# Kernel optimization log

Measured on AMD Instinct MI355X. Metric: run time of the kernel, lower is better.

## Reference

```python
import jax, jax.numpy as jnp
import numpy as np

EPS = 1e-5


def conv3d(x, w):
    # x: [N, C, D, H, W], w: [O, I, kD, kH, kW]; SAME padding emulates the
    # densified coordinate-expanding sparse conv on a fixed grid.
    return jax.lax.conv_general_dilated(
        x, w, window_strides=(1, 1, 1), padding='SAME',
        dimension_numbers=('NCDHW', 'OIDHW', 'NCDHW'))


def bn(x, gamma, beta, mean, var):
    # eval-mode batchnorm, fused scale/shift
    scale = gamma * jax.lax.rsqrt(var + EPS)          # [C]
    shift = beta - mean * scale                       # [C]
    return x * scale[None, :, None, None, None] + shift[None, :, None, None, None]


def setup_inputs() -> dict:
    key = jax.random.key(0)
    ks = jax.random.split(key, 20)
    C = 16
    D, H, W = 128, 128, 16

    def w(k, shape, fan):
        return jax.random.normal(k, shape, dtype=jnp.float32) / np.sqrt(fan)

    inp = {}
    inp['x'] = jax.random.normal(ks[0], (1, C, D, H, W), dtype=jnp.float32)
    inp['w1'] = w(ks[1], (C, C, 3, 3, 1), C * 9)
    inp['w2'] = w(ks[2], (C, C, 3, 3, 1), C * 9)
    inp['w3'] = w(ks[3], (C, C, 5, 5, 3), C * 75)
    inp['w4'] = w(ks[4], (C, C, 7, 7, 5), C * 245)
    inp['w5'] = w(ks[5], (C, C, 3, 3, 1), C * 9)
    inp['w6'] = w(ks[6], (C, C, 5, 5, 3), C * 75)
    inp['w7'] = w(ks[7], (C, C, 7, 7, 5), C * 245)
    inp['wch'] = w(ks[8], (C, C, 1, 1, 1), C)
    inp['wr1'] = w(ks[9], (C, C, 3, 3, 1), C * 9)
    inp['wr2'] = w(ks[10], (C, C, 5, 5, 3), C * 75)
    inp['wr3'] = w(ks[11], (C, C, 7, 7, 5), C * 245)
    # 10 BN layers: bn_1..bn_7 -> rows 0..6, bn_res_1..3 -> rows 7..9
    inp['bn_gamma'] = jax.random.uniform(ks[12], (10, C), dtype=jnp.float32) + 0.5
    inp['bn_beta'] = 0.1 * jax.random.normal(ks[13], (10, C), dtype=jnp.float32)
    inp['bn_mean'] = 0.1 * jax.random.normal(ks[14], (10, C), dtype=jnp.float32)
    inp['bn_var'] = jax.random.uniform(ks[15], (10, C), dtype=jnp.float32) + 0.5
    return inp


def reference(x, w1, w2, w3, w4, w5, w6, w7, wch, wr1, wr2, wr3,
              bn_gamma, bn_beta, bn_mean, bn_var):
    def cbn(h, w_, i):
        return bn(conv3d(h, w_), bn_gamma[i], bn_beta[i], bn_mean[i], bn_var[i])

    x1 = cbn(x, w1, 0)
    x2 = cbn(x1, w2, 1)
    x3 = cbn(x1, w3, 2)
    x4 = cbn(x1, w4, 3)
    t1 = jax.nn.relu(x2 + x3 + x4)
    x5 = cbn(t1, w5, 4)
    x6 = cbn(t1, w6, 5)
    x7 = cbn(t1, w7, 6)
    xs = jax.nn.relu(x1 + x2 + x3 + x4 + x5 + x6 + x7)
    y0 = conv3d(xs, wch)
    y1 = cbn(x, wr1, 7)
    y2 = cbn(x, wr2, 8)
    y3 = cbn(x, wr3, 9)
    return jax.nn.relu(x1 + y0 + y1 + y2 + y3)
```

## Files before the change

### kernel.cpp

```cpp
#include <hip/hip_runtime.h>
#include <hip/hip_bf16.h>

typedef __attribute__((ext_vector_type(8))) short short8;
typedef __attribute__((ext_vector_type(4))) short s16x4;
typedef __attribute__((ext_vector_type(4))) float f32x4;

constexpr int C  = 16;
constexpr int DD = 128, HH = 128, WW = 16;
constexpr int HW = HH * WW;
constexpr int SP = DD * HW;
constexpr int TOT = C * SP;

constexpr int WP_ = 20, HP_ = 134, DP_ = 134;
constexpr int ROWE   = WP_ * C;
constexpr int PLANEE = HP_ * ROWE;
constexpr int PADE   = DP_ * PLANEE;

using gas_ptr = const __attribute__((address_space(1))) void*;
using las_ptr = __attribute__((address_space(3))) void*;

constexpr int OFF_W1  = 0;
constexpr int OFF_WCH = 5 * 512;
constexpr int OFF_G0  = OFF_WCH + 512;
constexpr int OFF_G1  = OFF_G0 + 147 * 512;
constexpr int OFF_G2  = OFF_G1 + 147 * 512;
constexpr int WPK_TOT = OFF_G2 + 147 * 512;

constexpr int CONV_BUFSZ = 7 * 256 * 16;

__device__ __forceinline__ float bf16_to_f(short s)
{
    union { unsigned u; float f; } cv;
    cv.u = ((unsigned)(unsigned short)s) << 16;
    return cv.f;
}

template <int EP>
__device__ __forceinline__
void conv_core(int b, const short* __restrict__ xp, const short* __restrict__ wpk,
               const float* __restrict__ bias, float* __restrict__ F,
               short* __restrict__ P, char* __restrict__ smem)
{
    constexpr int KD = 7, KH = 7, KW = 5;
    constexpr int PH = 3;
    constexpr int KWP = 3;
    constexpr int NUP = (2 + KD - 1) / 2;
    constexpr int NB  = 8 + KH - 1;
    constexpr int NR  = 16 + 2 * PH;
    constexpr int NCHP = NR * 40;
    constexpr int NCH  = 2 * NCHP;

    const int dblk = b >> 3, hb = b & 7;
    const int d0   = dblk * 2;
    const int tid  = threadIdx.x;
    const int wid  = tid >> 6, lane = tid & 63;
    const int pid  = wid >> 1, m = wid & 1;
    const int l15  = lane & 15;
    const int cih  = (lane >> 4) & 1;
    const int tsel = lane >> 5;

    const char* xb = (const char*)xp;
    const char* wb = (const char*)wpk;
    const int hp0  = hb * 16;

    auto stage = [&](int buf, int up) {
#pragma unroll
        for (int it = 0; it < 7; ++it) {
            int chunk = it * 256 + tid;
            int cc = chunk < NCH ? chunk : NCH - 1;
            int pl = (cc >= NCHP) ? 1 : 0;
            int cp = cc - pl * NCHP;
            const char* g = xb
                + (size_t)((d0 + 2 * up + pl) * PLANEE + hp0 * ROWE) * 2
                + (size_t)cp * 16;
            void* l = (void*)(smem + buf * CONV_BUFSZ + (it * 256 + wid * 64) * 16);
            __builtin_amdgcn_global_load_lds((gas_ptr)g, (las_ptr)l, 16, 0, 0);
        }
    };

    f32x4 acc[2][8] = {};

    stage(0, 0);
#pragma unroll 1
    for (int up = 0; up < NUP; ++up) {
        const int cur = up & 1;
        if (up + 1 < NUP) {
            stage(cur ^ 1, up + 1);
            asm volatile("s_waitcnt vmcnt(7)" ::: "memory");
        } else {
            asm volatile("s_waitcnt vmcnt(0)" ::: "memory");
        }
        __builtin_amdgcn_s_barrier();

        const int u = 2 * up + m;
        const char* lb = smem + cur * CONV_BUFSZ + m * (NR * 640) + pid * 8 * 640;
#pragma unroll
        for (int kwp = 0; kwp < KWP; ++kwp) {
            const int kwa = 2 * kwp;
            const int kwb_ = (2 * kwp + 1 < KW) ? 2 * kwp + 1 : KW - 1;
            const unsigned laneoff =
                (unsigned)((l15 + (tsel ? kwb_ : kwa)) * 32 + cih * 16);

            short8 Bf[NB];
#pragma unroll
            for (int rB = 0; rB < NB; ++rB)
                Bf[rB] = *(const short8*)(lb + rB * 640 + laneoff);
            short8 Af[2][7];
#pragma unroll
            for (int ad = 0; ad < 2; ++ad) {
                const int kd = u - ad;
                if (kd < 0 || kd >= KD) continue;
#pragma unroll
                for (int kh = 0; kh < KH; ++kh)
                    Af[ad][kh] = *(const short8*)(
                        wb + (unsigned)(((kd * KH + kh) * KWP + kwp) * 1024 + lane * 16));
            }

            __builtin_amdgcn_s_setprio(1);
#pragma unroll
            for (int ad = 0; ad < 2; ++ad) {
                const int kd = u - ad;
                if (kd < 0 || kd >= KD) continue;
#pragma unroll
                for (int kh = 0; kh < KH; ++kh) {
#pragma unroll
                    for (int r = 0; r < 8; ++r)
                        acc[ad][r] = __builtin_amdgcn_mfma_f32_16x16x32_bf16(
                            Af[ad][kh], Bf[r + kh], acc[ad][r], 0, 0, 0);
                }
            }
            __builtin_amdgcn_s_setprio(0);
        }
        __builtin_amdgcn_s_barrier();
    }

    float* mlds = (float*)smem;
    if (m == 1) {
#pragma unroll
        for (int ad = 0; ad < 2; ++ad)
#pragma unroll
            for (int r = 0; r < 8; ++r)
                *(f32x4*)&mlds[(((pid * 2 + ad) * 8 + r) * 64 + lane) * 4] = acc[ad][r];
    }
    __syncthreads();
    if (m == 1) return;
#pragma unroll
    for (int ad = 0; ad < 2; ++ad)
#pragma unroll
        for (int r = 0; r < 8; ++r) {
            const f32x4 o = *(const f32x4*)&mlds[(((pid * 2 + ad) * 8 + r) * 64 + lane) * 4];
#pragma unroll
            for (int j = 0; j < 4; ++j) acc[ad][r][j] += o[j];
        }

    const int cb = (lane >> 4) * 4;
    const f32x4 bv = *(const f32x4*)(bias + cb);
    const int h0 = hb * 16 + pid * 8;
#pragma unroll
    for (int ad = 0; ad < 2; ++ad)
#pragma unroll
        for (int r = 0; r < 8; ++r) {
            const int d = d0 + ad, h = h0 + r;
            const unsigned fidx = (unsigned)(((d * HH + h) * WW + l15) * C + cb);
            f32x4 val;
#pragma unroll
            for (int j = 0; j < 4; ++j) val[j] = acc[ad][r][j] + bv[j];
            if (EP == 0) {
                *(f32x4*)(F + fidx) = val;
            } else if (EP == 2) {
                s16x4 sv;
#pragma unroll
                for (int j = 0; j < 4; ++j) {
                    __hip_bfloat16 hv = __float2bfloat16(fmaxf(val[j], 0.f));
                    sv[j] = *(short*)&hv;
                }
                *(s16x4*)(P + (size_t)(d + 3) * PLANEE + (h + 3) * ROWE
                          + (l15 + 2) * 16 + cb) = sv;
                *(f32x4*)(F + fidx) = val;
            } else {
                const f32x4 f2 = *(const f32x4*)(F + fidx);
                short* prow = P + (size_t)(d + 3) * PLANEE + (h + 3) * ROWE
                              + (l15 + 2) * 16 + cb;
                const s16x4 xv = *(const s16x4*)prow;
                s16x4 sv;
#pragma unroll
                for (int j = 0; j < 4; ++j) {
                    const float x1 = bf16_to_f(xv[j]);
                    __hip_bfloat16 hv = __float2bfloat16(fmaxf(x1 + val[j] + f2[j], 0.f));
                    sv[j] = *(short*)&hv;
                }
                *(s16x4*)prow = sv;
            }
        }
}

__device__ __forceinline__ int swz512(int b0)
{
    return (b0 & 7) * 64 + (b0 >> 3);
}

template <int EP>
__global__ __launch_bounds__(256, 2)
void conv_tile_lds(const short* __restrict__ xp, const short* __restrict__ wpk,
                   const float* __restrict__ bias, float* __restrict__ F,
                   short* __restrict__ P)
{
    __shared__ alignas(16) char smem[2 * CONV_BUFSZ];
    conv_core<EP>(swz512(blockIdx.x), xp, wpk, bias, F, P, smem);
}

__global__ __launch_bounds__(256, 2)
void conv_dual(const short* __restrict__ xpA, const short* __restrict__ wpkA,
               const float* __restrict__ biasA, float* __restrict__ FA,
               short* __restrict__ PA_,
               const short* __restrict__ xpB, const short* __restrict__ wpkB,
               const float* __restrict__ biasB, float* __restrict__ FB)
{
    __shared__ alignas(16) char smem[2 * CONV_BUFSZ];
    const int b0 = blockIdx.x;
    if (b0 < 512)
        conv_core<2>(swz512(b0), xpA, wpkA, biasA, FA, PA_, smem);
    else
        conv_core<0>(swz512(b0 - 512), xpB, wpkB, biasB, FB, nullptr, smem);
}

template <int KD, int KH, int KW, int NTAPS, bool WF, int PW>
__global__ __launch_bounds__(256, 4)
void conv_mfma(const short* __restrict__ xp, const short* __restrict__ wpk,
               const float* __restrict__ bn_g, const float* __restrict__ bn_b,
               const float* __restrict__ bn_m, const float* __restrict__ bn_v,
               int layer, float* __restrict__ F, short* __restrict__ P)
{
    constexpr int PD = (KD - 1) / 2, PH = (KH - 1) / 2, PW_ = (KW - 1) / 2;
    constexpr int NP = (NTAPS + 1) / 2;

    const int b    = blockIdx.x;
    const int d    = b >> 3, hb = b & 7;
    const int tid  = threadIdx.x;
    const int wid  = tid >> 6, lane = tid & 63;
    const int h0   = hb * 16 + wid * 4;

    const int l15  = lane & 15;
    const int cih  = (lane >> 4) & 1;
    const int tsel = lane >> 5;
    const unsigned laneoff = (unsigned)(l15 * 32 + cih * 16);

    unsigned off_r[4];
#pragma unroll
    for (int r = 0; r < 4; ++r) {
        const int h = h0 + r;
        off_r[r] = (unsigned)((((d + (3 - PD)) * HP_ + (h + (3 - PH))) * ROWE
                               + (2 - PW_) * C) * 2) + laneoff;
    }

    const char* xb = (const char*)xp;
    const char* wb = (const char*)wpk;

    f32x4 acc[4] = {};
#pragma unroll 2
    for (int p = 0; p < NP; ++p) {
        const int ta = 2 * p;
        const int tb = (2 * p + 1 < NTAPS) ? 2 * p + 1 : NTAPS - 1;
        const int kda = ta / (KH * KW), ra = ta % (KH * KW);
        const int kha = ra / KW,        kwa = ra % KW;
        const int kdb = tb / (KH * KW), rb = tb % (KH * KW);
        const int khb = rb / KW,        kwb = rb % KW;
        const unsigned toa = (unsigned)((kda * PLANEE + kha * ROWE + kwa * C) * 2);
        const unsigned tob = (unsigned)((kdb * PLANEE + khb * ROWE + kwb * C) * 2);
        const unsigned ts  = tsel ? tob : toa;

        const short8 a = *(const short8*)(wb + (unsigned)(p * 1024 + lane * 16));
#pragma unroll
        for (int r = 0; r < 4; ++r) {
            const short8 bf = *(const short8*)(xb + (off_r[r] + ts));
            acc[r] = __builtin_amdgcn_mfma_f32_16x16x32_bf16(a, bf, acc[r], 0, 0, 0);
        }
    }

    float sc[4], sh[4];
    const int cb = (lane >> 4) * 4;
    {
        const f32x4 g  = *(const f32x4*)(bn_g + layer * C + cb);
        const f32x4 be = *(const f32x4*)(bn_b + layer * C + cb);
        const f32x4 mm = *(const f32x4*)(bn_m + layer * C + cb);
        const f32x4 v  = *(const f32x4*)(bn_v + layer * C + cb);
#pragma unroll
        for (int j = 0; j < 4; ++j) { sc[j] = g[j] / sqrtf(v[j] + 1e-5f); sh[j] = be[j] - mm[j] * sc[j]; }
    }
#pragma unroll
    for (int r = 0; r < 4; ++r) {
        const int h = h0 + r;
        f32x4 val;
#pragma unroll
        for (int j = 0; j < 4; ++j) val[j] = acc[r][j] * sc[j] + sh[j];
        if (PW == 1) {
            s16x4 sv;
#pragma unroll
            for (int j = 0; j < 4; ++j) {
                __hip_bfloat16 hv = __float2bfloat16(val[j]);
                sv[j] = *(short*)&hv;
            }
            *(s16x4*)(P + (size_t)(d + 3) * PLANEE + (h + 3) * ROWE
                      + (l15 + 2) * 16 + cb) = sv;
        }
        if (WF) {
            float* dst = F + (unsigned)(((d * HH + h) * WW + l15) * C + cb);
            *(f32x4*)dst = val;
        }
    }
}

__global__ __launch_bounds__(256, 4)
void final_conv(const short* __restrict__ xsp, const short* __restrict__ wpk,
                const float* __restrict__ F1, float* __restrict__ out)
{
    const int b    = blockIdx.x;
    const int d    = b >> 3, hb = b & 7;
    const int tid  = threadIdx.x;
    const int wid  = tid >> 6, lane = tid & 63;
    const int h0   = hb * 16 + wid * 4;
    const int l15  = lane & 15;
    const int cih  = (lane >> 4) & 1;
    const int cb   = (lane >> 4) * 4;
    const unsigned laneoff = (unsigned)((l15 + 2) * 32 + cih * 16);

    const char* xb = (const char*)xsp;
    const short8 a = *(const short8*)((const char*)wpk + (unsigned)(lane * 16));

#pragma unroll
    for (int r = 0; r < 4; ++r) {
        const int h = h0 + r;
        const unsigned off = (unsigned)(((size_t)(d + 3) * PLANEE + (h + 3) * ROWE) * 2)
                             + laneoff;
        const short8 bf = *(const short8*)(xb + off);
        f32x4 acc = {};
        acc = __builtin_amdgcn_mfma_f32_16x16x32_bf16(a, bf, acc, 0, 0, 0);
        const f32x4 f1 = *(const f32x4*)(F1 + (unsigned)(((d * HH + h) * WW + l15) * C + cb));
#pragma unroll
        for (int j = 0; j < 4; ++j) {
            const float v = fmaxf(acc[j] + f1[j], 0.f);
            out[(unsigned)((cb + j) * SP + d * HW + h * WW + l15)] = v;
        }
    }
}

__global__ __launch_bounds__(256)
void pack_x(const float* __restrict__ x, short* __restrict__ xp,
            short* __restrict__ pa)
{
    const int b  = blockIdx.x;
    const int dp = b / HP_, hp = b % HP_;
    const int t  = threadIdx.x;
    const int d  = dp - 3, h = hp - 3;
    const bool inr = ((unsigned)d < (unsigned)DD) && ((unsigned)h < (unsigned)HH);
    short* row  = xp + (unsigned)(dp * PLANEE + hp * ROWE);
    short* rowp = pa + (unsigned)(dp * PLANEE + hp * ROWE);

    const int w = t & 15, ci = t >> 4;
    float v = 0.f;
    if (inr) v = x[ci * SP + d * HW + h * WW + w];
    __hip_bfloat16 hv = __float2bfloat16(v);
    row[(w + 2) * C + ci] = *(short*)&hv;
    if (t < 64) {
        const int pi = t >> 4;
        const int wp = (pi < 2) ? pi : (16 + pi);
        row[wp * C + (t & 15)] = 0;
    }
    if (!inr) {
        for (int i = t; i < ROWE; i += 256) rowp[i] = 0;
    } else if (t < 64) {
        const int pi = t >> 4;
        const int wp = (pi < 2) ? pi : (16 + pi);
        rowp[wp * C + (t & 15)] = 0;
    }
}

__global__ __launch_bounds__(256)
void pack_x2(const float* __restrict__ x, short* __restrict__ xp,
             short* __restrict__ pa, short* __restrict__ t1p)
{
    const int b  = blockIdx.x;
    const int dp = b / HP_, hp = b % HP_;
    const int t  = threadIdx.x;
    const int d  = dp - 3, h = hp - 3;
    const bool inr = ((unsigned)d < (unsigned)DD) && ((unsigned)h < (unsigned)HH);
    short* row  = xp  + (unsigned)(dp * PLANEE + hp * ROWE);
    short* rowp = pa  + (unsigned)(dp * PLANEE + hp * ROWE);
    short* rowt = t1p + (unsigned)(dp * PLANEE + hp * ROWE);

    const int w = t & 15, ci = t >> 4;
    float v = 0.f;
    if (inr) v = x[ci * SP + d * HW + h * WW + w];
    __hip_bfloat16 hv = __float2bfloat16(v);
    row[(w + 2) * C + ci] = *(short*)&hv;
    if (t < 64) {
        const int pi = t >> 4;
        const int wp = (pi < 2) ? pi : (16 + pi);
        row[wp * C + (t & 15)] = 0;
    }
    if (!inr) {
        for (int i = t; i < ROWE; i += 256) { rowp[i] = 0; rowt[i] = 0; }
    } else if (t < 64) {
        const int pi = t >> 4;
        const int wp = (pi < 2) ? pi : (16 + pi);
        rowp[wp * C + (t & 15)] = 0;
        rowt[wp * C + (t & 15)] = 0;
    }
}

__global__ __launch_bounds__(256)
void pack_small(const float* __restrict__ w1, const float* __restrict__ wch,
                short* __restrict__ dst)
{
    const int b = blockIdx.x;
    const int t = threadIdx.x;
    const int l = t >> 2, jj = t & 3;
    const int co = l & 15, cih = (l >> 4) & 1, tp = l >> 5;
    unsigned out = 0;
    if (b < 5) {
        const int tap = 2 * b + tp;
#pragma unroll
        for (int s = 0; s < 2; ++s) {
            const int ci = cih * 8 + jj * 2 + s;
            const float v = (tap < 9) ? w1[(co * C + ci) * 9 + tap] : 0.f;
            __hip_bfloat16 hv = __float2bfloat16(v);
            out |= ((unsigned)*(unsigned short*)&hv) << (16 * s);
        }
        ((unsigned*)(dst + OFF_W1))[b * 256 + l * 4 + jj] = out;
    } else {
#pragma unroll
        for (int s = 0; s < 2; ++s) {
            const int ci = cih * 8 + jj * 2 + s;
            const float v = (tp == 0) ? wch[co * C + ci] : 0.f;
            __hip_bfloat16 hv = __float2bfloat16(v);
            out |= ((unsigned)*(unsigned short*)&hv) << (16 * s);
        }
        ((unsigned*)(dst + OFF_WCH))[l * 4 + jj] = out;
    }
}

struct W9 { const float* p[9]; };

__global__ __launch_bounds__(256)
void pack_fused(W9 w, const float* __restrict__ w1,
                const float* __restrict__ bng, const float* __restrict__ bnb,
                const float* __restrict__ bnm, const float* __restrict__ bnv,
                short* __restrict__ dst, float* __restrict__ bias)
{
    constexpr int kDm[3] = {3, 5, 7}, kHm[3] = {3, 5, 7}, kWm[3] = {1, 3, 5};
    constexpr int KHWm[3] = {9, 75, 245};

    const int b = blockIdx.x;
    const int g = b / 147, pr = b % 147;
    const int row = pr / 3, kwp = pr % 3;
    const int kd = row / 7, kh = row % 7;
    const int t = threadIdx.x;
    const int l = t >> 2, jj = t & 3;
    const int co = l & 15, cih = (l >> 4) & 1, tp = l >> 5;
    const int kw = 2 * kwp + tp;

    unsigned out = 0;
#pragma unroll
    for (int s = 0; s < 2; ++s) {
        const int ci = cih * 8 + jj * 2 + s;
        float val = 0.f;
        if (kw < 5) {
#pragma unroll
            for (int m = 0; m < 3; ++m) {
                const int od = (7 - kDm[m]) / 2, oh = (7 - kHm[m]) / 2, ow = (5 - kWm[m]) / 2;
                const int rd = kd - od, rh = kh - oh, rw = kw - ow;
                if ((unsigned)rd < (unsigned)kDm[m] && (unsigned)rh < (unsigned)kHm[m]
                    && (unsigned)rw < (unsigned)kWm[m]) {
                    const int layer = g * 3 + m + 1;
                    const float sbn = bng[layer * C + co] / sqrtf(bnv[layer * C + co] + 1e-5f);
                    val += sbn * w.p[g * 3 + m][(co * C + ci) * KHWm[m]
                                               + (rd * kHm[m] + rh) * kWm[m] + rw];
                }
            }
            if (g == 2) {
                const int rd = kd - 2, rh = kh - 2, rw = kw - 2;
                if ((unsigned)rd < 3u && (unsigned)rh < 3u && rw == 0) {
                    const float sbn = bng[co] / sqrtf(bnv[co] + 1e-5f);
                    val += sbn * w1[(co * C + ci) * 9 + rd * 3 + rh];
                }
            }
        }
        __hip_bfloat16 hv = __float2bfloat16(val);
        out |= ((unsigned)*(unsigned short*)&hv) << (16 * s);
    }
    ((unsigned*)(dst + OFF_G0))[(g * 147 + pr) * 256 + l * 4 + jj] = out;

    if (pr == 0 && t < 16) {
        float bsum = 0.f;
#pragma unroll
        for (int m = 0; m < 3; ++m) {
            const int layer = g * 3 + m + 1;
            const float sbn = bng[layer * C + t] / sqrtf(bnv[layer * C + t] + 1e-5f);
            bsum += bnb[layer * C + t] - bnm[layer * C + t] * sbn;
        }
        if (g == 2) {
            const float sbn = bng[t] / sqrtf(bnv[t] + 1e-5f);
            bsum += bnb[t] - bnm[t] * sbn;
        }
        bias[g * 16 + t] = bsum;
    }
}

extern "C" void kernel_launch(void* const* d_in, const int* in_sizes, int n_in,
                              void* d_out, int out_size, void* d_ws, size_t ws_size,
                              hipStream_t stream)
{
    const float* x   = (const float*)d_in[0];
    const float* w1  = (const float*)d_in[1];
    const float* wch = (const float*)d_in[8];
    const float* bng = (const float*)d_in[12];
    const float* bnb = (const float*)d_in[13];
    const float* bnm = (const float*)d_in[14];
    const float* bnv = (const float*)d_in[15];

    W9 w9;
    w9.p[0] = (const float*)d_in[2];  w9.p[1] = (const float*)d_in[3];
    w9.p[2] = (const float*)d_in[4];  w9.p[3] = (const float*)d_in[5];
    w9.p[4] = (const float*)d_in[6];  w9.p[5] = (const float*)d_in[7];
    w9.p[6] = (const float*)d_in[9];  w9.p[7] = (const float*)d_in[10];
    w9.p[8] = (const float*)d_in[11];

    short* XP   = (short*)d_ws;
    short* PA   = XP + PADE;
    float* F1   = (float*)(PA + PADE);
    short* WPK  = (short*)(F1 + TOT);
    float* BIAS = (float*)(WPK + WPK_TOT);
    short* T1P  = (short*)(BIAS + 64);
    float* F2   = (float*)d_out;

    const size_t need = ((size_t)(3 * PADE + WPK_TOT) * 2)
                      + (size_t)TOT * 4 + 64 * 4;
    const bool merged = ws_size >= need;

    const dim3 blk(256);
    const dim3 pgrid(DP_ * HP_);
    const dim3 sgrid(DD * 8);
    const dim3 tgrid(512);

    if (merged) pack_x2<<<pgrid, blk, 0, stream>>>(x, XP, PA, T1P);
    else        pack_x<<<pgrid, blk, 0, stream>>>(x, XP, PA);
    pack_small<<<dim3(6), blk, 0, stream>>>(w1, wch, WPK);
    pack_fused<<<dim3(441), blk, 0, stream>>>(w9, w1, bng, bnb, bnm, bnv, WPK, BIAS);

    conv_mfma<3,3,1,9,false,1><<<sgrid, blk, 0, stream>>>(
        XP, WPK + OFF_W1, bng, bnb, bnm, bnv, 0, nullptr, PA);

    if (merged) {
        conv_dual<<<dim3(1024), blk, 0, stream>>>(
            PA, WPK + OFF_G0, BIAS + 0, F2, T1P,
            XP, WPK + OFF_G2, BIAS + 32, F1);
        conv_tile_lds<3><<<tgrid, blk, 0, stream>>>(T1P, WPK + OFF_G1, BIAS + 16, F2, PA);
    } else {
        conv_tile_lds<0><<<tgrid, blk, 0, stream>>>(XP, WPK + OFF_G2, BIAS + 32, F1, nullptr);
        conv_tile_lds<2><<<tgrid, blk, 0, stream>>>(PA, WPK + OFF_G0, BIAS + 0, F2, XP);
        conv_tile_lds<3><<<tgrid, blk, 0, stream>>>(XP, WPK + OFF_G1, BIAS + 16, F2, PA);
    }
    final_conv<<<sgrid, blk, 0, stream>>>(PA, WPK + OFF_WCH, F1, (float*)d_out);

    (void)in_sizes; (void)n_in; (void)out_size; (void)ws_size;
}
```

Baseline: 127.4 us.

## Halve conv tile height and block size to 128 threads for more blocks

```diff
diff --git a/kernel.cpp b/kernel.cpp
--- a/kernel.cpp
+++ b/kernel.cpp
@@ -26,7 +26,7 @@
 constexpr int OFF_G2  = OFF_G1 + 147 * 512;
 constexpr int WPK_TOT = OFF_G2 + 147 * 512;
 
-constexpr int CONV_BUFSZ = 7 * 256 * 16;
+constexpr int CONV_BUFSZ = 9 * 128 * 16;
 
 __device__ __forceinline__ float bf16_to_f(short s)
 {
@@ -42,38 +42,37 @@
                short* __restrict__ P, char* __restrict__ smem)
 {
     constexpr int KD = 7, KH = 7, KW = 5;
-    constexpr int PH = 3;
     constexpr int KWP = 3;
     constexpr int NUP = (2 + KD - 1) / 2;
     constexpr int NB  = 8 + KH - 1;
-    constexpr int NR  = 16 + 2 * PH;
+    constexpr int NR  = 14;
     constexpr int NCHP = NR * 40;
     constexpr int NCH  = 2 * NCHP;
-
-    const int dblk = b >> 3, hb = b & 7;
+    constexpr int STIT = 9;
+
+    const int dblk = b >> 4, hb = b & 15;
     const int d0   = dblk * 2;
     const int tid  = threadIdx.x;
-    const int wid  = tid >> 6, lane = tid & 63;
-    const int pid  = wid >> 1, m = wid & 1;
+    const int m    = tid >> 6, lane = tid & 63;
     const int l15  = lane & 15;
     const int cih  = (lane >> 4) & 1;
     const int tsel = lane >> 5;
 
     const char* xb = (const char*)xp;
     const char* wb = (const char*)wpk;
-    const int hp0  = hb * 16;
+    const int hp0  = hb * 8;
 
     auto stage = [&](int buf, int up) {
 #pragma unroll
-        for (int it = 0; it < 7; ++it) {
-            int chunk = it * 256 + tid;
+        for (int it = 0; it < STIT; ++it) {
+            int chunk = it * 128 + tid;
             int cc = chunk < NCH ? chunk : NCH - 1;
             int pl = (cc >= NCHP) ? 1 : 0;
             int cp = cc - pl * NCHP;
             const char* g = xb
                 + (size_t)((d0 + 2 * up + pl) * PLANEE + hp0 * ROWE) * 2
                 + (size_t)cp * 16;
-            void* l = (void*)(smem + buf * CONV_BUFSZ + (it * 256 + wid * 64) * 16);
+            void* l = (void*)(smem + buf * CONV_BUFSZ + (it * 128 + m * 64) * 16);
             __builtin_amdgcn_global_load_lds((gas_ptr)g, (las_ptr)l, 16, 0, 0);
         }
     };
@@ -86,14 +85,14 @@
         const int cur = up & 1;
         if (up + 1 < NUP) {
             stage(cur ^ 1, up + 1);
-            asm volatile("s_waitcnt vmcnt(7)" ::: "memory");
+            asm volatile("s_waitcnt vmcnt(9)" ::: "memory");
         } else {
             asm volatile("s_waitcnt vmcnt(0)" ::: "memory");
         }
         __builtin_amdgcn_s_barrier();
 
         const int u = 2 * up + m;
-        const char* lb = smem + cur * CONV_BUFSZ + m * (NR * 640) + pid * 8 * 640;
+        const char* lb = smem + cur * CONV_BUFSZ + m * (NR * 640);
 #pragma unroll
         for (int kwp = 0; kwp < KWP; ++kwp) {
             const int kwa = 2 * kwp;
@@ -140,7 +139,7 @@
         for (int ad = 0; ad < 2; ++ad)
 #pragma unroll
             for (int r = 0; r < 8; ++r)
-                *(f32x4*)&mlds[(((pid * 2 + ad) * 8 + r) * 64 + lane) * 4] = acc[ad][r];
+                *(f32x4*)&mlds[((ad * 8 + r) * 64 + lane) * 4] = acc[ad][r];
     }
     __syncthreads();
     if (m == 1) return;
@@ -148,14 +147,14 @@
     for (int ad = 0; ad < 2; ++ad)
 #pragma unroll
         for (int r = 0; r < 8; ++r) {
-            const f32x4 o = *(const f32x4*)&mlds[(((pid * 2 + ad) * 8 + r) * 64 + lane) * 4];
+            const f32x4 o = *(const f32x4*)&mlds[((ad * 8 + r) * 64 + lane) * 4];
 #pragma unroll
             for (int j = 0; j < 4; ++j) acc[ad][r][j] += o[j];
         }
 
     const int cb = (lane >> 4) * 4;
     const f32x4 bv = *(const f32x4*)(bias + cb);
-    const int h0 = hb * 16 + pid * 8;
+    const int h0 = hb * 8;
 #pragma unroll
     for (int ad = 0; ad < 2; ++ad)
 #pragma unroll
@@ -194,22 +193,22 @@
         }
 }
 
-__device__ __forceinline__ int swz512(int b0)
-{
-    return (b0 & 7) * 64 + (b0 >> 3);
+__device__ __forceinline__ int swz1024(int b0)
+{
+    return (b0 & 7) * 128 + (b0 >> 3);
 }
 
 template <int EP>
-__global__ __launch_bounds__(256, 2)
+__global__ __launch_bounds__(128, 2)
 void conv_tile_lds(const short* __restrict__ xp, const short* __restrict__ wpk,
                    const float* __restrict__ bias, float* __restrict__ F,
                    short* __restrict__ P)
 {
     __shared__ alignas(16) char smem[2 * CONV_BUFSZ];
-    conv_core<EP>(swz512(blockIdx.x), xp, wpk, bias, F, P, smem);
-}
-
-__global__ __launch_bounds__(256, 2)
+    conv_core<EP>(swz1024(blockIdx.x), xp, wpk, bias, F, P, smem);
+}
+
+__global__ __launch_bounds__(128, 2)
 void conv_dual(const short* __restrict__ xpA, const short* __restrict__ wpkA,
                const float* __restrict__ biasA, float* __restrict__ FA,
                short* __restrict__ PA_,
@@ -218,10 +217,10 @@
 {
     __shared__ alignas(16) char smem[2 * CONV_BUFSZ];
     const int b0 = blockIdx.x;
-    if (b0 < 512)
-        conv_core<2>(swz512(b0), xpA, wpkA, biasA, FA, PA_, smem);
+    if (b0 < 1024)
+        conv_core<2>(swz1024(b0), xpA, wpkA, biasA, FA, PA_, smem);
     else
-        conv_core<0>(swz512(b0 - 512), xpB, wpkB, biasB, FB, nullptr, smem);
+        conv_core<0>(swz1024(b0 - 1024), xpB, wpkB, biasB, FB, nullptr, smem);
 }
 
 template <int KD, int KH, int KW, int NTAPS, bool WF, int PW>
@@ -537,10 +536,10 @@
                       + (size_t)TOT * 4 + 64 * 4;
     const bool merged = ws_size >= need;
 
-    const dim3 blk(256);
+    const dim3 blk(256), blk128(128);
     const dim3 pgrid(DP_ * HP_);
     const dim3 sgrid(DD * 8);
-    const dim3 tgrid(512);
+    const dim3 tgrid(1024);
 
     if (merged) pack_x2<<<pgrid, blk, 0, stream>>>(x, XP, PA, T1P);
     else        pack_x<<<pgrid, blk, 0, stream>>>(x, XP, PA);
@@ -551,14 +550,14 @@
         XP, WPK + OFF_W1, bng, bnb, bnm, bnv, 0, nullptr, PA);
 
     if (merged) {
-        conv_dual<<<dim3(1024), blk, 0, stream>>>(
+        conv_dual<<<dim3(2048), blk128, 0, stream>>>(
             PA, WPK + OFF_G0, BIAS + 0, F2, T1P,
             XP, WPK + OFF_G2, BIAS + 32, F1);
-        conv_tile_lds<3><<<tgrid, blk, 0, stream>>>(T1P, WPK + OFF_G1, BIAS + 16, F2, PA);
+        conv_tile_lds<3><<<tgrid, blk128, 0, stream>>>(T1P, WPK + OFF_G1, BIAS + 16, F2, PA);
     } else {
-        conv_tile_lds<0><<<tgrid, blk, 0, stream>>>(XP, WPK + OFF_G2, BIAS + 32, F1, nullptr);
-        conv_tile_lds<2><<<tgrid, blk, 0, stream>>>(PA, WPK + OFF_G0, BIAS + 0, F2, XP);
-        conv_tile_lds<3><<<tgrid, blk, 0, stream>>>(XP, WPK + OFF_G1, BIAS + 16, F2, PA);
+        conv_tile_lds<0><<<tgrid, blk128, 0, stream>>>(XP, WPK + OFF_G2, BIAS + 32, F1, nullptr);
+        conv_tile_lds<2><<<tgrid, blk128, 0, stream>>>(PA, WPK + OFF_G0, BIAS + 0, F2, XP);
+        conv_tile_lds<3><<<tgrid, blk128, 0, stream>>>(XP, WPK + OFF_G1, BIAS + 16, F2, PA);
     }
     final_conv<<<sgrid, blk, 0, stream>>>(PA, WPK + OFF_WCH, F1, (float*)d_out);
 
```

After: 135.9 us. 1.07x slower.
